# Performance work log

Measured on AMD Instinct MI355X. Metric: run time of the kernel, lower is better.

The kernel has to match this reference:

```python
import jax, jax.numpy as jnp
import numpy as np

N = 50000
E = 500000
H = 128


def setup_inputs() -> dict:
    key = jax.random.key(0)
    ks = jax.random.split(key, 7)
    x = jax.random.normal(ks[0], (N, 4, H), dtype=jnp.float32)
    edge_index = jax.random.randint(ks[1], (2, E), 0, N, dtype=jnp.int64)
    s = 1.0 / np.sqrt(H)
    W_s_rel = jax.random.normal(ks[2], (H, H), dtype=jnp.float32) * s
    W_s_root = jax.random.normal(ks[3], (H, H), dtype=jnp.float32) * s
    b_s_root = jax.random.normal(ks[4], (H,), dtype=jnp.float32) * s
    W_v_rel = jax.random.normal(ks[5], (H, H), dtype=jnp.float32) * s
    W_v_root = jax.random.normal(ks[6], (H, H), dtype=jnp.float32) * s
    return {"x": x, "edge_index": edge_index, "W_s_rel": W_s_rel,
            "W_s_root": W_s_root, "b_s_root": b_s_root,
            "W_v_rel": W_v_rel, "W_v_root": W_v_root}


def reference(x, edge_index, W_s_rel, W_s_root, b_s_root, W_v_rel, W_v_root):
    # x: (N, 4, H); channel 0 is scalar, channels 1:4 are a 3-vector per feature
    scalar = x[:, 0, :]          # (N, H)
    vector = x[:, 1:, :]         # (N, 3, H)
    row, col = edge_index[0], edge_index[1]
    n = scalar.shape[0]

    # Per-edge messages: gather source (col) features, project with rel weights
    scalar_msg = scalar[col] @ W_s_rel.T                     # (E, H)
    vector_msg = jnp.einsum('evh,oh->evo', vector[col], W_v_rel)  # (E, 3, H)

    # Scatter-add into destination (row) nodes
    scalar_agg = jax.ops.segment_sum(scalar_msg, row, num_segments=n)
    vector_agg = jax.ops.segment_sum(vector_msg, row, num_segments=n)

    scalar_out = scalar @ W_s_root.T + b_s_root + scalar_agg          # (N, H)
    vector_out = jnp.einsum('nvh,oh->nvo', vector, W_v_root) + vector_agg  # (N, 3, H)

    return jnp.concatenate([scalar_out[:, None, :], vector_out], axis=1)  # (N, 4, H)
```

## Files before the change

### kernel.cpp

```cpp
#include <hip/hip_runtime.h>


typedef short bfrag __attribute__((ext_vector_type(8)));
typedef float cfrag __attribute__((ext_vector_type(16)));
typedef float f4v  __attribute__((ext_vector_type(4)));

__device__ __forceinline__ short f2bf(float f) {
    unsigned u = __builtin_bit_cast(unsigned, f);
    u += 0x7fff + ((u >> 16) & 1);
    return (short)(u >> 16);
}
__device__ __forceinline__ float bf2f(short s) {
    unsigned u = ((unsigned)(unsigned short)s) << 16;
    return __builtin_bit_cast(float, u);
}
__device__ __forceinline__ bfrag pack8(float4 lo, float4 hi) {
    bfrag r;
    r[0] = f2bf(lo.x); r[1] = f2bf(lo.y); r[2] = f2bf(lo.z); r[3] = f2bf(lo.w);
    r[4] = f2bf(hi.x); r[5] = f2bf(hi.y); r[6] = f2bf(hi.z); r[7] = f2bf(hi.w);
    return r;
}
__device__ __forceinline__ bfrag pack8v(f4v lo, f4v hi) {
    bfrag r;
    r[0] = f2bf(lo[0]); r[1] = f2bf(lo[1]); r[2] = f2bf(lo[2]); r[3] = f2bf(lo[3]);
    r[4] = f2bf(hi[0]); r[5] = f2bf(hi[1]); r[6] = f2bf(hi[2]); r[7] = f2bf(hi[3]);
    return r;
}

__global__ __launch_bounds__(256) void prep_kernel(
    const float* __restrict__ x, short* __restrict__ xbf, long long total8,
    const float* __restrict__ w0, const float* __restrict__ w1,
    const float* __restrict__ w2, const float* __restrict__ w3,
    short* __restrict__ wbf,
    const int* __restrict__ ei, int* __restrict__ counts, int E,
    int convB)
{
    int b = blockIdx.x;
    if (b < convB) {
        long long i = (long long)b * 256 + threadIdx.x;
        if (i >= total8) return;
        f4v lo = __builtin_nontemporal_load((const f4v*)(x + i * 8));
        f4v hi = __builtin_nontemporal_load((const f4v*)(x + i * 8 + 4));
        *(bfrag*)(xbf + i * 8) = pack8v(lo, hi);
    } else if (b < convB + 32) {
        int i = (b - convB) * 256 + threadIdx.x;
        int j = i * 8;
        int m = j >> 14, off = j & 16383;
        const float* src = (m == 0) ? w0 : (m == 1) ? w1 : (m == 2) ? w2 : w3;
        float4 lo = *(const float4*)(src + off);
        float4 hi = *(const float4*)(src + off + 4);
        *(bfrag*)(wbf + j) = pack8(lo, hi);
    } else {
        int e = (b - convB - 32) * 256 + threadIdx.x;
        if (e < E) atomicAdd(&counts[ei[e]], 1);
    }
}

__global__ __launch_bounds__(1024) void scan_local_kernel(
    const int* __restrict__ counts, int* __restrict__ offsets,
    int* __restrict__ blocksums, int N)
{
    __shared__ int wsum[16];
    const int tid = threadIdx.x, lane = tid & 63, wid = tid >> 6;
    int i = blockIdx.x * 1024 + tid;
    int v = (i < N) ? counts[i] : 0;
    int incl = v;
    #pragma unroll
    for (int off = 1; off < 64; off <<= 1) {
        int t = __shfl_up(incl, off, 64);
        if (lane >= off) incl += t;
    }
    if (lane == 63) wsum[wid] = incl;
    __syncthreads();
    if (wid == 0) {
        int ws = (lane < 16) ? wsum[lane] : 0;
        int wincl = ws;
        #pragma unroll
        for (int off = 1; off < 16; off <<= 1) {
            int t = __shfl_up(wincl, off, 64);
            if (lane >= off) wincl += t;
        }
        if (lane < 16) wsum[lane] = wincl - ws;
    }
    __syncthreads();
    int excl = incl - v + wsum[wid];
    if (i < N) offsets[i] = excl;
    if (tid == 1023) blocksums[blockIdx.x] = excl + v;
}

__global__ __launch_bounds__(1024) void scan_fix_kernel(
    int* __restrict__ offsets, int* __restrict__ cursor,
    const int* __restrict__ blocksums, int nb, int N, int E)
{
    __shared__ int pref;
    if (threadIdx.x < 64) {
        int lane = threadIdx.x;
        int v = (lane < nb) ? blocksums[lane] : 0;
        int incl = v;
        #pragma unroll
        for (int off = 1; off < 64; off <<= 1) {
            int t = __shfl_up(incl, off, 64);
            if (lane >= off) incl += t;
        }
        if (lane == (int)blockIdx.x) pref = incl - v;
    }
    __syncthreads();
    int i = blockIdx.x * 1024 + threadIdx.x;
    if (i < N) {
        int v = offsets[i] + pref;
        offsets[i] = v;
        cursor[i] = v;
    }
    if (i == 0) offsets[N] = E;
}

__global__ __launch_bounds__(256) void bin_kernel(
    const int* __restrict__ ei, int* __restrict__ cursor,
    int* __restrict__ bins, int E)
{
    int e = blockIdx.x * 256 + threadIdx.x;
    if (e < E) {
        int row = ei[e], col = ei[E + e];
        int pos = atomicAdd(&cursor[row], 1);
        bins[pos] = col;
    }
}

template<int XBF>
__global__ __launch_bounds__(256) void fused_agg_mfma(
    const float* __restrict__ x, const short* __restrict__ xbf,
    const int* __restrict__ offsets, const int* __restrict__ bins,
    float* __restrict__ out, const short* __restrict__ wbf,
    const float* __restrict__ b_s, int Nn)
{
    __shared__ short atile[32 * 512];
    const int tid  = threadIdx.x;
    const int wid  = tid >> 6;
    const int lane = tid & 63;
    const int n0   = blockIdx.x * 32;

    const int cl   = lane >> 4;
    const int slot = lane & 15;
    #pragma unroll 1
    for (int i = 0; i < 8; i++) {
        const int m = wid * 8 + i;
        const int n = n0 + m;
        float acc[8] = {0, 0, 0, 0, 0, 0, 0, 0};
        if (n < Nn) {
            const int beg = offsets[n], end = offsets[n + 1];
            int e = beg;
            if (XBF) {
                for (; e + 8 <= end; e += 8) {
                    int cc[8];
                    #pragma unroll
                    for (int q = 0; q < 8; q++) cc[q] = bins[e + q];
                    bfrag v[8];
                    #pragma unroll
                    for (int q = 0; q < 8; q++)
                        v[q] = *(const bfrag*)(xbf + (size_t)cc[q] * 512 + lane * 8);
                    #pragma unroll
                    for (int j = 0; j < 8; j++)
                        acc[j] += ((bf2f(v[0][j]) + bf2f(v[1][j])) +
                                   (bf2f(v[2][j]) + bf2f(v[3][j]))) +
                                  ((bf2f(v[4][j]) + bf2f(v[5][j])) +
                                   (bf2f(v[6][j]) + bf2f(v[7][j])));
                }
                for (; e + 4 <= end; e += 4) {
                    int c4[4];
                    #pragma unroll
                    for (int q = 0; q < 4; q++) c4[q] = bins[e + q];
                    bfrag v[4];
                    #pragma unroll
                    for (int q = 0; q < 4; q++)
                        v[q] = *(const bfrag*)(xbf + (size_t)c4[q] * 512 + lane * 8);
                    #pragma unroll
                    for (int j = 0; j < 8; j++)
                        acc[j] += (bf2f(v[0][j]) + bf2f(v[1][j])) +
                                  (bf2f(v[2][j]) + bf2f(v[3][j]));
                }
                for (; e < end; e++) {
                    int cc1 = bins[e];
                    bfrag v = *(const bfrag*)(xbf + (size_t)cc1 * 512 + lane * 8);
                    #pragma unroll
                    for (int j = 0; j < 8; j++) acc[j] += bf2f(v[j]);
                }
            } else {
                for (; e < end; e++) {
                    int cc1 = bins[e];
                    float4 l = *(const float4*)(x + (size_t)cc1 * 512 + lane * 8);
                    float4 h = *(const float4*)(x + (size_t)cc1 * 512 + lane * 8 + 4);
                    acc[0] += l.x; acc[1] += l.y; acc[2] += l.z; acc[3] += l.w;
                    acc[4] += h.x; acc[5] += h.y; acc[6] += h.z; acc[7] += h.w;
                }
            }
        }
        const int boff = m * 1024 + cl * 256 + ((slot * 16) ^ ((m & 15) << 4));
        *(bfrag*)((char*)atile + boff) =
            pack8(make_float4(acc[0], acc[1], acc[2], acc[3]),
                  make_float4(acc[4], acc[5], acc[6], acc[7]));
    }

    const int c   = wid;
    const int l31 = lane & 31;
    const int kg  = lane >> 5;
    int mA = n0 + l31; if (mA >= Nn) mA = Nn - 1;
    const size_t arow = ((size_t)mA * 4 + c) * 128;
    bfrag a0[8];
    #pragma unroll
    for (int ks = 0; ks < 8; ks++) {
        const int k0 = ks * 16 + kg * 8;
        if (XBF) {
            a0[ks] = *(const bfrag*)(xbf + arow + k0);
        } else {
            float4 lo = *(const float4*)(x + arow + k0);
            float4 hi = *(const float4*)(x + arow + k0 + 4);
            a0[ks] = pack8(lo, hi);
        }
    }

    __syncthreads();

    const short* wroot = wbf + ((c == 0) ? 0 : 2) * 16384;
    const short* wrel  = wbf + ((c == 0) ? 1 : 3) * 16384;

    cfrag acc4[4];
    #pragma unroll
    for (int t = 0; t < 4; t++)
        #pragma unroll
        for (int r = 0; r < 16; r++) acc4[t][r] = 0.f;

    __builtin_amdgcn_s_setprio(1);
    #pragma unroll
    for (int ks = 0; ks < 8; ks++) {
        const int k0 = ks * 16 + kg * 8;
        const int rboff = l31 * 1024 + c * 256 + ((k0 * 2) ^ ((l31 & 15) << 4));
        bfrag a1 = *(const bfrag*)((const char*)atile + rboff);
        #pragma unroll
        for (int t = 0; t < 4; t++) {
            bfrag b0 = *(const bfrag*)(wroot + (size_t)(t * 32 + l31) * 128 + k0);
            acc4[t] = __builtin_amdgcn_mfma_f32_32x32x16_bf16(a0[ks], b0, acc4[t], 0, 0, 0);
            bfrag b1 = *(const bfrag*)(wrel + (size_t)(t * 32 + l31) * 128 + k0);
            acc4[t] = __builtin_amdgcn_mfma_f32_32x32x16_bf16(a1, b1, acc4[t], 0, 0, 0);
        }
    }
    __builtin_amdgcn_s_setprio(0);

    float bv[4] = {0.f, 0.f, 0.f, 0.f};
    if (c == 0) {
        #pragma unroll
        for (int t = 0; t < 4; t++) bv[t] = b_s[t * 32 + l31];
    }

    #pragma unroll
    for (int t = 0; t < 4; t++) {
        #pragma unroll
        for (int r = 0; r < 16; r++) {
            int row = (r & 3) + 8 * (r >> 2) + 4 * kg;
            int node = n0 + row;
            if (node < Nn)
                __builtin_nontemporal_store(
                    acc4[t][r] + bv[t],
                    out + ((size_t)node * 4 + c) * 128 + t * 32 + l31);
        }
    }
}

extern "C" void kernel_launch(void* const* d_in, const int* in_sizes, int n_in,
                              void* d_out, int out_size, void* d_ws, size_t ws_size,
                              hipStream_t stream) {
    const float* x        = (const float*)d_in[0];
    const int*   ei       = (const int*)d_in[1];
    const float* W_s_rel  = (const float*)d_in[2];
    const float* W_s_root = (const float*)d_in[3];
    const float* b_s_root = (const float*)d_in[4];
    const float* W_v_rel  = (const float*)d_in[5];
    const float* W_v_root = (const float*)d_in[6];
    float* out = (float*)d_out;

    int N = in_sizes[0] / 512;
    int E = in_sizes[1] / 2;

    size_t ints_bytes = ((size_t)(3 * N + 1) + E + 64) * sizeof(int);
    size_t wbf_bytes  = 65536 * sizeof(short);
    size_t xbf_bytes  = (size_t)N * 512 * sizeof(short);
    bool use_bf = (ws_size >= wbf_bytes + xbf_bytes + ints_bytes);

    short* wbf = (short*)d_ws;
    short* xbf = wbf + 65536;
    int* counts = use_bf ? (int*)(xbf + (size_t)N * 512) : (int*)xbf;
    int* offsets   = counts + N;
    int* cursor    = offsets + N + 1;
    int* bins      = cursor + N;
    int* blocksums = bins + E;

    int nb = (N + 1023) / 1024;
    long long total8 = (long long)N * 64;
    int convB = use_bf ? (int)((total8 + 255) / 256) : 0;
    int nh = (E + 255) / 256;

    hipMemsetAsync(counts, 0, (size_t)N * sizeof(int), stream);
    prep_kernel<<<convB + 32 + nh, 256, 0, stream>>>(
        x, xbf, total8, W_s_root, W_s_rel, W_v_root, W_v_rel, wbf,
        ei, counts, E, convB);
    scan_local_kernel<<<nb, 1024, 0, stream>>>(counts, offsets, blocksums, N);
    scan_fix_kernel<<<nb, 1024, 0, stream>>>(offsets, cursor, blocksums, nb, N, E);
    bin_kernel<<<(E + 255) / 256, 256, 0, stream>>>(ei, cursor, bins, E);

    if (use_bf) {
        fused_agg_mfma<1><<<(N + 31) / 32, 256, 0, stream>>>(
            x, xbf, offsets, bins, out, wbf, b_s_root, N);
    } else {
        fused_agg_mfma<0><<<(N + 31) / 32, 256, 0, stream>>>(
            x, nullptr, offsets, bins, out, wbf, b_s_root, N);
    }
}
```

Measured before the change: 379.2 us.

## Merge scan fixup, binning and x-to-bf16 conversion into one kernel

Removes the separate scan_fix kernel by having scan_local write block-local cursors and letting each binning thread add the block prefix (recomputed per block from blocksums) on the fly. The binning, offset fixup and the x bf16 conversion now run as block ranges of a single launch, and the conversion moves out of the first prep kernel. This cuts one kernel launch and serialization point, and lets the bandwidth-heavy conversion overlap with the atomic-bound binning. Each block redoes a small 64-lane scan, and the design relies on nb being at most 64.

```diff
diff --git a/kernel.cpp b/kernel.cpp
--- a/kernel.cpp
+++ b/kernel.cpp
@@ -27,23 +27,15 @@
     return r;
 }
 
-__global__ __launch_bounds__(256) void prep_kernel(
-    const float* __restrict__ x, short* __restrict__ xbf, long long total8,
+__global__ __launch_bounds__(256) void prep0_kernel(
     const float* __restrict__ w0, const float* __restrict__ w1,
     const float* __restrict__ w2, const float* __restrict__ w3,
     short* __restrict__ wbf,
-    const int* __restrict__ ei, int* __restrict__ counts, int E,
-    int convB)
+    const int* __restrict__ ei, int* __restrict__ counts, int E)
 {
     int b = blockIdx.x;
-    if (b < convB) {
-        long long i = (long long)b * 256 + threadIdx.x;
-        if (i >= total8) return;
-        f4v lo = __builtin_nontemporal_load((const f4v*)(x + i * 8));
-        f4v hi = __builtin_nontemporal_load((const f4v*)(x + i * 8 + 4));
-        *(bfrag*)(xbf + i * 8) = pack8v(lo, hi);
-    } else if (b < convB + 32) {
-        int i = (b - convB) * 256 + threadIdx.x;
+    if (b < 32) {
+        int i = b * 256 + threadIdx.x;
         int j = i * 8;
         int m = j >> 14, off = j & 16383;
         const float* src = (m == 0) ? w0 : (m == 1) ? w1 : (m == 2) ? w2 : w3;
@@ -51,14 +43,14 @@
         float4 hi = *(const float4*)(src + off + 4);
         *(bfrag*)(wbf + j) = pack8(lo, hi);
     } else {
-        int e = (b - convB - 32) * 256 + threadIdx.x;
+        int e = (b - 32) * 256 + threadIdx.x;
         if (e < E) atomicAdd(&counts[ei[e]], 1);
     }
 }
 
 __global__ __launch_bounds__(1024) void scan_local_kernel(
     const int* __restrict__ counts, int* __restrict__ offsets,
-    int* __restrict__ blocksums, int N)
+    int* __restrict__ cursor, int* __restrict__ blocksums, int N)
 {
     __shared__ int wsum[16];
     const int tid = threadIdx.x, lane = tid & 63, wid = tid >> 6;
@@ -84,45 +76,51 @@
     }
     __syncthreads();
     int excl = incl - v + wsum[wid];
-    if (i < N) offsets[i] = excl;
+    if (i < N) { offsets[i] = excl; cursor[i] = excl; }
     if (tid == 1023) blocksums[blockIdx.x] = excl + v;
 }
 
-__global__ __launch_bounds__(1024) void scan_fix_kernel(
-    int* __restrict__ offsets, int* __restrict__ cursor,
-    const int* __restrict__ blocksums, int nb, int N, int E)
+__global__ __launch_bounds__(256) void mega_kernel(
+    const int* __restrict__ ei, int* __restrict__ cursor,
+    int* __restrict__ bins, int E,
+    int* __restrict__ offsets, const int* __restrict__ blocksums,
+    int nb, int N,
+    const float* __restrict__ x, short* __restrict__ xbf, long long total8,
+    int nbin, int nfix)
 {
-    __shared__ int pref;
-    if (threadIdx.x < 64) {
-        int lane = threadIdx.x;
-        int v = (lane < nb) ? blocksums[lane] : 0;
-        int incl = v;
-        #pragma unroll
-        for (int off = 1; off < 64; off <<= 1) {
-            int t = __shfl_up(incl, off, 64);
-            if (lane >= off) incl += t;
-        }
-        if (lane == (int)blockIdx.x) pref = incl - v;
-    }
-    __syncthreads();
-    int i = blockIdx.x * 1024 + threadIdx.x;
-    if (i < N) {
-        int v = offsets[i] + pref;
-        offsets[i] = v;
-        cursor[i] = v;
-    }
-    if (i == 0) offsets[N] = E;
-}
-
-__global__ __launch_bounds__(256) void bin_kernel(
-    const int* __restrict__ ei, int* __restrict__ cursor,
-    int* __restrict__ bins, int E)
-{
-    int e = blockIdx.x * 256 + threadIdx.x;
-    if (e < E) {
-        int row = ei[e], col = ei[E + e];
-        int pos = atomicAdd(&cursor[row], 1);
-        bins[pos] = col;
+    int b = blockIdx.x;
+    if (b < nbin + nfix) {
+        __shared__ int pref[64];
+        if (threadIdx.x < 64) {
+            int lane = threadIdx.x;
+            int v = (lane < nb) ? blocksums[lane] : 0;
+            int incl = v;
+            #pragma unroll
+            for (int off = 1; off < 64; off <<= 1) {
+                int t = __shfl_up(incl, off, 64);
+                if (lane >= off) incl += t;
+            }
+            pref[lane] = incl - v;
+        }
+        __syncthreads();
+        if (b < nbin) {
+            int e = b * 256 + threadIdx.x;
+            if (e < E) {
+                int row = ei[e], col = ei[E + e];
+                int pos = atomicAdd(&cursor[row], 1) + pref[row >> 10];
+                bins[pos] = col;
+            }
+        } else {
+            int i = (b - nbin) * 256 + threadIdx.x;
+            if (i < N) offsets[i] += pref[i >> 10];
+            else if (i == N) offsets[i] = E;
+        }
+    } else {
+        long long i = (long long)(b - nbin - nfix) * 256 + threadIdx.x;
+        if (i >= total8) return;
+        f4v lo = __builtin_nontemporal_load((const f4v*)(x + i * 8));
+        f4v hi = __builtin_nontemporal_load((const f4v*)(x + i * 8 + 4));
+        *(bfrag*)(xbf + i * 8) = pack8v(lo, hi);
     }
 }
 
@@ -295,16 +293,18 @@
 
     int nb = (N + 1023) / 1024;
     long long total8 = (long long)N * 64;
-    int convB = use_bf ? (int)((total8 + 255) / 256) : 0;
-    int nh = (E + 255) / 256;
+    int nconv = use_bf ? (int)((total8 + 255) / 256) : 0;
+    int nbin  = (E + 255) / 256;
+    int nfix  = (N + 1 + 255) / 256;
+    int nh    = nbin;
 
     hipMemsetAsync(counts, 0, (size_t)N * sizeof(int), stream);
-    prep_kernel<<<convB + 32 + nh, 256, 0, stream>>>(
-        x, xbf, total8, W_s_root, W_s_rel, W_v_root, W_v_rel, wbf,
-        ei, counts, E, convB);
-    scan_local_kernel<<<nb, 1024, 0, stream>>>(counts, offsets, blocksums, N);
-    scan_fix_kernel<<<nb, 1024, 0, stream>>>(offsets, cursor, blocksums, nb, N, E);
-    bin_kernel<<<(E + 255) / 256, 256, 0, stream>>>(ei, cursor, bins, E);
+    prep0_kernel<<<32 + nh, 256, 0, stream>>>(
+        W_s_root, W_s_rel, W_v_root, W_v_rel, wbf, ei, counts, E);
+    scan_local_kernel<<<nb, 1024, 0, stream>>>(counts, offsets, cursor, blocksums, N);
+    mega_kernel<<<nbin + nfix + nconv, 256, 0, stream>>>(
+        ei, cursor, bins, E, offsets, blocksums, nb, N,
+        x, xbf, total8, nbin, nfix);
 
     if (use_bf) {
         fused_agg_mfma<1><<<(N + 31) / 32, 256, 0, stream>>>(
```

After: 377.8 us. About the same (-0.4%).
